# Kernel optimization log

Hardware: AMD Instinct MI355X
Metric: run time of the kernel (lower is better)

Reference implementation:

```python
import jax, jax.numpy as jnp
import numpy as np

M, N, P, D = 256, 512, 24, 8


def _se(X, Y):
    # base squared-exponential kernel between point sets: exp(-0.5*||x-y||^2)
    d2 = jnp.sum(X * X, -1)[:, None] + jnp.sum(Y * Y, -1)[None, :] - 2.0 * (X @ Y.T)
    return jnp.exp(-0.5 * jnp.maximum(d2, 0.0))


def _pairwise_dist(X1, A1, X2, A2):
    # vectorized version of the original double loop over metric(f1, f2)
    m, p, d = X1.shape
    n, q, _ = X2.shape
    # cross terms: C[i,j] = a_i @ K(x_i, x_j) @ a_j   (one big Gram, batched quadratic form)
    K12 = _se(X1.reshape(m * p, d), X2.reshape(n * q, d)).reshape(m, p, n, q)
    C = jnp.einsum('iu,iujv,jv->ij', A1, K12, A2)
    # self terms: s_i = a_i @ K(x_i, x_i) @ a_i (computed ONCE, not per inner iteration)
    s1 = jnp.einsum('iu,iuv,iv->i', A1, jax.vmap(_se)(X1, X1), A1)
    s2 = jnp.einsum('ju,juv,jv->j', A2, jax.vmap(_se)(X2, X2), A2)
    d2 = s1[:, None] + s2[None, :] - 2.0 * C
    # matches lax.cond(d2 <= 0, 0.0, sqrt(d2))
    return jnp.sqrt(jnp.maximum(d2, 0.0))


def _kernel(rho, X1, A1, X2, A2):
    # SquaredExponential profile applied to d / sqrt(rho)
    u = _pairwise_dist(X1, A1, X2, A2) / jnp.sqrt(rho)
    return jnp.exp(-0.5 * u * u)


def setup_inputs() -> dict:
    key = jax.random.key(0)
    k = jax.random.split(key, 5)
    return {
        'X_test': jax.random.normal(k[0], (M, P, D), jnp.float32),
        'A_test': 0.2 * jax.random.normal(k[1], (M, P), jnp.float32),
        'X_obs': jax.random.normal(k[2], (N, P, D), jnp.float32),
        'A_obs': 0.2 * jax.random.normal(k[3], (N, P), jnp.float32),
        'observed_ys': jax.random.normal(k[4], (N,), jnp.float32),
        'rho': jnp.asarray(4.0, jnp.float32),
        'g': jnp.asarray(1e-3, jnp.float32),
        'nu': jnp.asarray(1.0, jnp.float32),
        'b': jnp.asarray(0.0, jnp.float32),
    }


def reference(X_test, A_test, X_obs, A_obs, observed_ys, rho, g, nu, b):
    # predict(): Kxx, Kox, Koo then gp_posterior
    Kxx = nu * _kernel(rho, X_test, A_test, X_test, A_test)          # [M, M]
    Kox = nu * _kernel(rho, X_obs, A_obs, X_test, A_test)            # [N, M]
    Koo = nu * (_kernel(rho, X_obs, A_obs, X_obs, A_obs) + g * jnp.eye(N, dtype=X_obs.dtype))

    gain = jnp.linalg.solve(Koo, Kox).T                              # [M, N]
    mean = b + gain @ (observed_ys - b)                              # [M]
    cov = Kxx - gain @ Kox                                           # [M, M]
    Kbx = jnp.ones((1, N), Koo.dtype) @ gain.T                       # [1, M]
    # 1^T Koo^{-1} 1 == inv(Koo).sum(), computed via a solve
    Koo_inv_sum = jnp.linalg.solve(Koo, jnp.ones((N,), Koo.dtype)).sum()
    cov = cov + (1.0 - Kbx).T @ (1.0 - Kbx) / Koo_inv_sum
    # stack mean on top of cov -> [M+1, M]
    return jnp.concatenate([mean[None, :], cov], axis=0)
```

## Files before the change

kernel.cpp:

```cpp
#include <hip/hip_runtime.h>
#include <cmath>

#define M 256
#define N 512
#define P 24
#define D 8

__global__ __launch_bounds__(64) void self_kernel(const float* __restrict__ X_test,
                                                  const float* __restrict__ A_test,
                                                  const float* __restrict__ X_obs,
                                                  const float* __restrict__ A_obs,
                                                  float* __restrict__ s1,
                                                  float* __restrict__ s2,
                                                  float* __restrict__ atT,
                                                  float* __restrict__ atO,
                                                  double* __restrict__ Bc) {
    const int bid = blockIdx.x;
    const int lane = threadIdx.x;
    if (bid == M + N) {
#pragma unroll
        for (int t = 0; t < 8; ++t) Bc[(size_t)256 * 512 + 64 * t + lane] = 1.0;
        return;
    }
    const float* X; const float* A; float* s; float* at; int i;
    if (bid < M) { X = X_test; A = A_test; s = s1; at = atT; i = bid; }
    else         { X = X_obs;  A = A_obs;  s = s2; at = atO; i = bid - M; }
    const float* Xi = X + (size_t)i * P * D;
    const float* Ai = A + (size_t)i * P;
    float acc = 0.f;
#pragma unroll
    for (int t = 0; t < 9; ++t) {
        int idx = lane + 64 * t;
        int u = idx / 24;
        int v = idx - u * 24;
        const float* xu = Xi + u * D;
        const float* xv = Xi + v * D;
        float d2 = 0.f;
#pragma unroll
        for (int d = 0; d < D; ++d) { float df = xu[d] - xv[d]; d2 = fmaf(df, df, d2); }
        acc = fmaf(Ai[u] * Ai[v], __expf(-0.5f * d2), acc);
    }
#pragma unroll
    for (int off = 1; off < 64; off <<= 1) acc += __shfl_xor(acc, off, 64);
    if (lane == 0) s[i] = acc;
    if (lane < 24) {
        const float* xp = Xi + lane * D;
        float q = 0.f;
#pragma unroll
        for (int d = 0; d < D; ++d) q = fmaf(xp[d], xp[d], q);
        at[(size_t)i * P + lane] = Ai[lane] * __expf(-0.5f * q);
    }
}

__global__ __launch_bounds__(128) void gram_kernel(
    const float* __restrict__ Xt, const float* __restrict__ atT, const float* __restrict__ s1,
    const float* __restrict__ Xo, const float* __restrict__ atO, const float* __restrict__ s2,
    const float* __restrict__ rho_p, const float* __restrict__ nu_p, const float* __restrict__ g_p,
    float* __restrict__ Kox, float* __restrict__ Kxx, double* __restrict__ Koo,
    double* __restrict__ Bc) {
    const int mode = blockIdx.z;
    const int it = blockIdx.x, jt = blockIdx.y;
    const float *X1, *AT1, *S1, *X2, *AT2, *S2;
    if (mode == 0) {
        if (jt > 2 * it + 1) return;
        X1 = Xo; AT1 = atO; S1 = s2; X2 = Xo; AT2 = atO; S2 = s2;
    } else if (mode == 1) {
        if (jt >= 32) return;
        X1 = Xo; AT1 = atO; S1 = s2; X2 = Xt; AT2 = atT; S2 = s1;
    } else {
        if (it >= 16 || jt >= 32 || jt < 2 * it) return;
        X1 = Xt; AT1 = atT; S1 = s1; X2 = Xt; AT2 = atT; S2 = s1;
    }
    const int i0 = it * 16, j0 = jt * 8;
    const int tid = threadIdx.x;
    const int il = tid >> 3, uc = tid & 7;
    const int i = i0 + il;

    __shared__ __align__(16) float X2s[8 * 192];
    __shared__ float A2s[8 * 24];
    __shared__ float S2s[8];
    {
        const float4* gx = (const float4*)(X2 + (size_t)j0 * 192);
        float4* lx = (float4*)X2s;
        for (int idx = tid; idx < 8 * 48; idx += 128) lx[idx] = gx[idx];
        for (int idx = tid; idx < 8 * 24; idx += 128) A2s[idx] = AT2[(size_t)j0 * 24 + idx];
        if (tid < 8) S2s[tid] = S2[j0 + tid];
    }
    __syncthreads();

    float x1r[3][8], at1r[3];
#pragma unroll
    for (int ss = 0; ss < 3; ++ss) {
        const float* p = X1 + ((size_t)i * P + uc * 3 + ss) * D;
#pragma unroll
        for (int d = 0; d < D; ++d) x1r[ss][d] = p[d];
        at1r[ss] = AT1[(size_t)i * P + uc * 3 + ss];
    }
    const float s1i = S1[i];
    const float rho = rho_p[0], nu = nu_p[0], g = g_p[0];

    for (int jj = 0; jj < 8; ++jj) {
        const float* xb = X2s + jj * 192;
        float e0 = 0.f, e1 = 0.f, e2 = 0.f;
#pragma unroll 4
        for (int v = 0; v < 24; ++v) {
            const float4 q0 = ((const float4*)(xb + v * 8))[0];
            const float4 q1 = ((const float4*)(xb + v * 8))[1];
            float x2r[8];
            x2r[0] = q0.x; x2r[1] = q0.y; x2r[2] = q0.z; x2r[3] = q0.w;
            x2r[4] = q1.x; x2r[5] = q1.y; x2r[6] = q1.z; x2r[7] = q1.w;
            const float w2 = A2s[jj * 24 + v];
            float d0 = 0.f, d1 = 0.f, d2 = 0.f;
#pragma unroll
            for (int dd = 0; dd < 8; ++dd) {
                d0 = fmaf(x1r[0][dd], x2r[dd], d0);
                d1 = fmaf(x1r[1][dd], x2r[dd], d1);
                d2 = fmaf(x1r[2][dd], x2r[dd], d2);
            }
            e0 = fmaf(w2, __expf(d0), e0);
            e1 = fmaf(w2, __expf(d1), e1);
            e2 = fmaf(w2, __expf(d2), e2);
        }
        float acc = at1r[0] * e0;
        acc = fmaf(at1r[1], e1, acc);
        acc = fmaf(at1r[2], e2, acc);
        acc += __shfl_xor(acc, 1, 8);
        acc += __shfl_xor(acc, 2, 8);
        acc += __shfl_xor(acc, 4, 8);
        if (uc == 0) {
            const int j = j0 + jj;
            float d2p = fmaxf(s1i + S2s[jj] - 2.f * acc, 0.f);
            float kv = __expf(-0.5f * d2p / rho);
            if (mode == 0) {
                if (j <= i) Koo[(size_t)i * 512 + j] = (double)(nu * (kv + ((i == j) ? g : 0.f)));
            } else if (mode == 1) {
                float val = nu * kv;
                Kox[(size_t)i * 256 + j] = val;
                Bc[(size_t)j * 512 + i] = (double)val;
            } else {
                float val = nu * kv;
                if (j >= i) {
                    Kxx[(size_t)i * 256 + j] = val;
                    if (j > i) Kxx[(size_t)j * 256 + i] = val;
                }
            }
        }
    }
}

#define NT_(p) (7 - (p))
#define NS_(p) ((7 - (p)) * (8 - (p)) / 2)

__device__ __forceinline__ void spin_ge(int* f, int target) {
    if (threadIdx.x == 0) {
        while (__hip_atomic_load(f, __ATOMIC_ACQUIRE, __HIP_MEMORY_SCOPE_AGENT) < target)
            __builtin_amdgcn_s_sleep(2);
    }
    __syncthreads();
}

__global__ __launch_bounds__(256) void chol_kernel(double* __restrict__ A,
                                                   double* __restrict__ LT,
                                                   double* __restrict__ Dinv,
                                                   double* __restrict__ DinvT,
                                                   int* __restrict__ flags) {
    int* fdone = flags;
    int* tdone = flags + 8;
    int* s00   = flags + 16;
    int* scol0 = flags + 24;
    int* sall  = flags + 32;

    int bid = blockIdx.x, p = 0, rem = bid;
    for (;; ++p) {
        int tot = 1 + NT_(p) + NS_(p);
        if (rem < tot) break;
        rem -= tot;
    }
    const int k0 = p * 64;
    const int tid = threadIdx.x;

    __shared__ double smem[2 * 64 * 65 + 3 * 16 * 17];

    if (rem == 0) {
        double (*sA)[65] = (double(*)[65])smem;
        double (*sX)[65] = (double(*)[65])(smem + 64 * 65);
        double* sW = smem + 2 * 64 * 65;
        if (p > 0) spin_ge(&s00[p - 1], 1);
        for (int idx = tid; idx < 4096; idx += 256) {
            int r = idx >> 6, c = idx & 63;
            sA[r][c] = (c <= r) ? A[(size_t)(k0 + r) * 512 + k0 + c] : 0.0;
            sX[r][c] = 0.0;
        }
        __syncthreads();
        for (int q = 0; q < 4; ++q) {
            const int b0 = 16 * q;
            if (tid < 64) {
                for (int k = 0; k < 15; ++k) {
                    double inv = 1.0 / sA[b0 + k][b0 + k];
#pragma unroll
                    for (int t = 0; t < 4; ++t) {
                        int idx = tid + 64 * t, r = idx >> 4, c = idx & 15;
                        if (r > k && c > k && c <= r)
                            sA[b0 + r][b0 + c] -= sA[b0 + r][b0 + k] * sA[b0 + c][b0 + k] * inv;
                    }
                    asm volatile("" ::: "memory");
                }
                double dq = (tid < 16) ? sqrt(sA[b0 + tid][b0 + tid]) : 1.0;
                asm volatile("" ::: "memory");
#pragma unroll
                for (int t = 0; t < 4; ++t) {
                    int idx = tid + 64 * t, r = idx >> 4, c = idx & 15;
                    double dcol = __shfl(dq, c, 64);
                    if (c <= r) sA[b0 + r][b0 + c] = (r == c) ? dcol : sA[b0 + r][b0 + c] / dcol;
                }
                asm volatile("" ::: "memory");
                int c = tid >> 2, qd = tid & 3;
                if (qd == 0) sX[b0 + c][b0 + c] = 1.0 / sA[b0 + c][b0 + c];
                asm volatile("" ::: "memory");
                for (int r = 1; r < 16; ++r) {
                    double partial = 0.0;
                    for (int t = c + qd; t < r; t += 4)
                        partial = fma(sA[b0 + r][b0 + t], sX[b0 + t][b0 + c], partial);
                    partial += __shfl_xor(partial, 1, 4);
                    partial += __shfl_xor(partial, 2, 4);
                    if (qd == 0 && r > c)
                        sX[b0 + r][b0 + c] = -partial / sA[b0 + r][b0 + r];
                    asm volatile("" ::: "memory");
                }
            }
            __syncthreads();
            if (q < 3) {
                const int nrows = 48 - b0;
                const int cells = nrows * 16;
                double tv[3];
#pragma unroll
                for (int ii = 0; ii < 3; ++ii) {
                    int idx = tid + 256 * ii;
                    tv[ii] = 0.0;
                    if (idx < cells) {
                        int a = b0 + 16 + (idx >> 4), cc = idx & 15;
                        double acc = 0.0;
                        for (int t = 0; t <= cc; ++t)
                            acc = fma(sA[a][b0 + t], sX[b0 + cc][b0 + t], acc);
                        tv[ii] = acc;
                    }
                }
                __syncthreads();
#pragma unroll
                for (int ii = 0; ii < 3; ++ii) {
                    int idx = tid + 256 * ii;
                    if (idx < cells) {
                        int a = b0 + 16 + (idx >> 4), cc = idx & 15;
                        sA[a][b0 + cc] = tv[ii];
                    }
                }
                __syncthreads();
                for (int idx = tid; idx < nrows * nrows; idx += 256) {
                    int r = b0 + 16 + idx / nrows, cc = b0 + 16 + idx % nrows;
                    if (cc <= r) {
                        double acc = 0.0;
#pragma unroll
                        for (int t = 0; t < 16; ++t)
                            acc = fma(sA[r][b0 + t], sA[cc][b0 + t], acc);
                        sA[r][cc] -= acc;
                    }
                }
                __syncthreads();
            }
        }
        for (int d = 1; d <= 3; ++d) {
            __syncthreads();
            int npairs = 4 - d;
            for (int i2 = tid; i2 < npairs * 256; i2 += 256) {
                int pr = i2 >> 8, cell = i2 & 255, r = cell >> 4, c = cell & 15;
                int qc = pr, qr = pr + d;
                double w = 0.0;
                for (int t = 16 * qc; t < 16 * qr; ++t)
                    w = fma(sA[16 * qr + r][t], sX[t][16 * qc + c], w);
                sW[pr * 272 + r * 17 + c] = w;
            }
            __syncthreads();
            for (int i2 = tid; i2 < npairs * 256; i2 += 256) {
                int pr = i2 >> 8, cell = i2 & 255, r = cell >> 4, c = cell & 15;
                int qc = pr, qr = pr + d;
                double x = 0.0;
                for (int t = 0; t <= r; ++t)
                    x = fma(sX[16 * qr + r][16 * qr + t], sW[pr * 272 + t * 17 + c], x);
                sX[16 * qr + r][16 * qc + c] = -x;
            }
        }
        __syncthreads();
        for (int idx = tid; idx < 4096; idx += 256) {
            int r = idx >> 6, c = idx & 63;
            if (c <= r) {
                double lv = sA[r][c];
                A[(size_t)(k0 + r) * 512 + k0 + c] = lv;
                LT[(size_t)(k0 + c) * 512 + k0 + r] = lv;
            }
            double xv = sX[r][c];
            Dinv[(size_t)p * 4096 + idx] = xv;
            DinvT[(size_t)p * 4096 + (size_t)c * 64 + r] = xv;
        }
        __syncthreads();
        if (tid == 0) __hip_atomic_fetch_add(&fdone[p], 1, __ATOMIC_RELEASE, __HIP_MEMORY_SCOPE_AGENT);

    } else if (rem <= NT_(p)) {
        double (*sA)[65] = (double(*)[65])smem;
        double (*sB)[65] = (double(*)[65])(smem + 64 * 65);
        const int b = rem - 1;
        const int i0 = k0 + 64 + b * 64;
        if (p > 0) spin_ge(&scol0[p - 1], NT_(p - 1));
        spin_ge(&fdone[p], 1);
        for (int idx = tid; idx < 4096; idx += 256) {
            int r = idx >> 6, c = idx & 63;
            sA[r][c] = A[(size_t)(i0 + r) * 512 + k0 + c];
            sB[r][c] = DinvT[(size_t)p * 4096 + idx];
        }
        __syncthreads();
        const int tx = tid & 15, ty = tid >> 4;
        double acc[4][4] = {};
        for (int t = 0; t < 64; ++t) {
            double a0 = sA[4 * ty + 0][t], a1 = sA[4 * ty + 1][t];
            double a2 = sA[4 * ty + 2][t], a3 = sA[4 * ty + 3][t];
            double b0 = sB[t][4 * tx + 0], b1 = sB[t][4 * tx + 1];
            double b2 = sB[t][4 * tx + 2], b3 = sB[t][4 * tx + 3];
            acc[0][0] = fma(a0, b0, acc[0][0]); acc[0][1] = fma(a0, b1, acc[0][1]);
            acc[0][2] = fma(a0, b2, acc[0][2]); acc[0][3] = fma(a0, b3, acc[0][3]);
            acc[1][0] = fma(a1, b0, acc[1][0]); acc[1][1] = fma(a1, b1, acc[1][1]);
            acc[1][2] = fma(a1, b2, acc[1][2]); acc[1][3] = fma(a1, b3, acc[1][3]);
            acc[2][0] = fma(a2, b0, acc[2][0]); acc[2][1] = fma(a2, b1, acc[2][1]);
            acc[2][2] = fma(a2, b2, acc[2][2]); acc[2][3] = fma(a2, b3, acc[2][3]);
            acc[3][0] = fma(a3, b0, acc[3][0]); acc[3][1] = fma(a3, b1, acc[3][1]);
            acc[3][2] = fma(a3, b2, acc[3][2]); acc[3][3] = fma(a3, b3, acc[3][3]);
        }
#pragma unroll
        for (int r = 0; r < 4; ++r)
#pragma unroll
            for (int c = 0; c < 4; ++c) {
                A[(size_t)(i0 + 4 * ty + r) * 512 + k0 + 4 * tx + c] = acc[r][c];
                LT[(size_t)(k0 + 4 * tx + c) * 512 + i0 + 4 * ty + r] = acc[r][c];
            }
        __syncthreads();
        if (tid == 0) __hip_atomic_fetch_add(&tdone[p], 1, __ATOMIC_RELEASE, __HIP_MEMORY_SCOPE_AGENT);

    } else {
        double (*Li)[65] = (double(*)[65])smem;
        double (*Lj)[65] = (double(*)[65])(smem + 64 * 65);
        int s = rem - 1 - NT_(p);
        int bi = 0;
        while (s >= (bi + 1) * (bi + 2) / 2) ++bi;
        int bj = s - bi * (bi + 1) / 2;
        const int i0 = k0 + 64 + bi * 64, j0 = k0 + 64 + bj * 64;
        if (p > 0) spin_ge(&sall[p - 1], NS_(p - 1));
        spin_ge(&tdone[p], NT_(p));
        for (int idx = tid; idx < 4096; idx += 256) {
            int r = idx >> 6, c = idx & 63;
            Li[r][c] = A[(size_t)(i0 + r) * 512 + k0 + c];
            Lj[r][c] = A[(size_t)(j0 + r) * 512 + k0 + c];
        }
        __syncthreads();
        const int tx = tid & 15, ty = tid >> 4;
        double acc[4][4] = {};
        for (int t = 0; t < 64; ++t) {
            double a0 = Li[4 * ty + 0][t], a1 = Li[4 * ty + 1][t];
            double a2 = Li[4 * ty + 2][t], a3 = Li[4 * ty + 3][t];
            double b0 = Lj[4 * tx + 0][t], b1 = Lj[4 * tx + 1][t];
            double b2 = Lj[4 * tx + 2][t], b3 = Lj[4 * tx + 3][t];
            acc[0][0] = fma(a0, b0, acc[0][0]); acc[0][1] = fma(a0, b1, acc[0][1]);
            acc[0][2] = fma(a0, b2, acc[0][2]); acc[0][3] = fma(a0, b3, acc[0][3]);
            acc[1][0] = fma(a1, b0, acc[1][0]); acc[1][1] = fma(a1, b1, acc[1][1]);
            acc[1][2] = fma(a1, b2, acc[1][2]); acc[1][3] = fma(a1, b3, acc[1][3]);
            acc[2][0] = fma(a2, b0, acc[2][0]); acc[2][1] = fma(a2, b1, acc[2][1]);
            acc[2][2] = fma(a2, b2, acc[2][2]); acc[2][3] = fma(a2, b3, acc[2][3]);
            acc[3][0] = fma(a3, b0, acc[3][0]); acc[3][1] = fma(a3, b1, acc[3][1]);
            acc[3][2] = fma(a3, b2, acc[3][2]); acc[3][3] = fma(a3, b3, acc[3][3]);
        }
#pragma unroll
        for (int r = 0; r < 4; ++r)
#pragma unroll
            for (int c = 0; c < 4; ++c) {
                int gi = i0 + 4 * ty + r, gj = j0 + 4 * tx + c;
                if (bi != bj || gj <= gi) A[(size_t)gi * 512 + gj] -= acc[r][c];
            }
        __syncthreads();
        if (tid == 0) {
            __hip_atomic_fetch_add(&sall[p], 1, __ATOMIC_RELEASE, __HIP_MEMORY_SCOPE_AGENT);
            if (bj == 0) __hip_atomic_fetch_add(&scol0[p], 1, __ATOMIC_RELEASE, __HIP_MEMORY_SCOPE_AGENT);
            if (bi == 0 && bj == 0) __hip_atomic_fetch_add(&s00[p], 1, __ATOMIC_RELEASE, __HIP_MEMORY_SCOPE_AGENT);
        }
    }
}

__global__ __launch_bounds__(64) void solve_kernel(const double* __restrict__ L,
                                                   const double* __restrict__ U,
                                                   const double* __restrict__ Dinv,
                                                   const double* __restrict__ DinvT,
                                                   double* __restrict__ B,
                                                   const float* __restrict__ ys,
                                                   const float* __restrict__ b_p,
                                                   float* __restrict__ out,
                                                   double* __restrict__ kbx,
                                                   double* __restrict__ Sp) {
    const int c = blockIdx.x, lane = threadIdx.x;
    double* col = B + (size_t)c * 512;
    __shared__ double y[512];
    __shared__ double z[512];
    __shared__ double v[64];
    double breg[8];
#pragma unroll
    for (int k = 0; k < 8; ++k) breg[k] = col[64 * k + lane];
    for (int k = 0; k < 8; ++k) {
        const double* row = L + (size_t)(64 * k + lane) * 512;
        double acc = 0.0;
        for (int j = 0; j < 64 * k; j += 8) {
            double2 l0 = *(const double2*)(row + j + 0);
            double2 l1 = *(const double2*)(row + j + 2);
            double2 l2 = *(const double2*)(row + j + 4);
            double2 l3 = *(const double2*)(row + j + 6);
            acc = fma(l0.x, y[j + 0], acc); acc = fma(l0.y, y[j + 1], acc);
            acc = fma(l1.x, y[j + 2], acc); acc = fma(l1.y, y[j + 3], acc);
            acc = fma(l2.x, y[j + 4], acc); acc = fma(l2.y, y[j + 5], acc);
            acc = fma(l3.x, y[j + 6], acc); acc = fma(l3.y, y[j + 7], acc);
        }
        v[lane] = breg[k] - acc;
        __syncthreads();
        const double* Dk = DinvT + (size_t)k * 4096;
        double yr = 0.0;
#pragma unroll 8
        for (int t = 0; t < 64; ++t) yr = fma(Dk[t * 64 + lane], v[t], yr);
        y[64 * k + lane] = yr;
        __syncthreads();
    }
    for (int k = 7; k >= 0; --k) {
        const double* row = U + (size_t)(64 * k + lane) * 512;
        double acc = 0.0;
        for (int j = 64 * (k + 1); j < 512; j += 8) {
            double2 l0 = *(const double2*)(row + j + 0);
            double2 l1 = *(const double2*)(row + j + 2);
            double2 l2 = *(const double2*)(row + j + 4);
            double2 l3 = *(const double2*)(row + j + 6);
            acc = fma(l0.x, z[j + 0], acc); acc = fma(l0.y, z[j + 1], acc);
            acc = fma(l1.x, z[j + 2], acc); acc = fma(l1.y, z[j + 3], acc);
            acc = fma(l2.x, z[j + 4], acc); acc = fma(l2.y, z[j + 5], acc);
            acc = fma(l3.x, z[j + 6], acc); acc = fma(l3.y, z[j + 7], acc);
        }
        v[lane] = y[64 * k + lane] - acc;
        __syncthreads();
        const double* Dk = Dinv + (size_t)k * 4096;
        double zr = 0.0;
#pragma unroll 8
        for (int t = 0; t < 64; ++t) zr = fma(Dk[t * 64 + lane], v[t], zr);
        z[64 * k + lane] = zr;
        __syncthreads();
    }
    const double b = (double)b_p[0];
    double s0 = 0.0, s1 = 0.0;
#pragma unroll
    for (int k = 0; k < 8; ++k) {
        int n = 64 * k + lane;
        double zv = z[n];
        col[n] = zv;
        s0 += zv;
        s1 = fma(zv, (double)ys[n] - b, s1);
    }
#pragma unroll
    for (int off = 1; off < 64; off <<= 1) {
        s0 += __shfl_xor(s0, off, 64);
        s1 += __shfl_xor(s1, off, 64);
    }
    if (lane == 0) {
        if (c < 256) { out[c] = (float)(b + s1); kbx[c] = s0; }
        else Sp[0] = s0;
    }
}

__global__ __launch_bounds__(256) void cov_kernel(const double* __restrict__ Z,
                                                  const float* __restrict__ Kox,
                                                  const float* __restrict__ Kxx,
                                                  const double* __restrict__ kbx,
                                                  const double* __restrict__ Sp,
                                                  float* __restrict__ out) {
    const int bj = blockIdx.x, bi = blockIdx.y;
    const int tx = threadIdx.x & 15, ty = threadIdx.x >> 4;
    const int i = bi * 16 + ty, j = bj * 16 + tx;
    __shared__ double sZ[16][17];
    __shared__ float sK[16][17];
    double acc = 0.0;
    for (int kt = 0; kt < 32; ++kt) {
        sZ[ty][tx] = Z[(size_t)i * 512 + kt * 16 + tx];
        sK[ty][tx] = Kox[(size_t)(kt * 16 + ty) * 256 + j];
        __syncthreads();
#pragma unroll
        for (int t = 0; t < 16; ++t) acc = fma(sZ[ty][t], (double)sK[t][tx], acc);
        __syncthreads();
    }
    const double S = Sp[0];
    const double corr = (1.0 - kbx[i]) * (1.0 - kbx[j]) / S;
    out[(size_t)(1 + i) * 256 + j] = (float)((double)Kxx[(size_t)i * 256 + j] - acc + corr);
}

extern "C" void kernel_launch(void* const* d_in, const int* in_sizes, int n_in,
                              void* d_out, int out_size, void* d_ws, size_t ws_size,
                              hipStream_t stream) {
    const float* X_test = (const float*)d_in[0];
    const float* A_test = (const float*)d_in[1];
    const float* X_obs  = (const float*)d_in[2];
    const float* A_obs  = (const float*)d_in[3];
    const float* ys     = (const float*)d_in[4];
    const float* rho_p  = (const float*)d_in[5];
    const float* g_p    = (const float*)d_in[6];
    const float* nu_p   = (const float*)d_in[7];
    const float* b_p    = (const float*)d_in[8];
    float* out = (float*)d_out;
    char* ws = (char*)d_ws;

    double* Koo  = (double*)(ws + 0);
    double* LT   = (double*)(ws + 2097152);
    double* Bc   = (double*)(ws + 4194304);
    float*  Kox  = (float*) (ws + 5246976);
    float*  Kxx  = (float*) (ws + 5771264);
    float*  s1v  = (float*) (ws + 6033408);
    float*  s2v  = (float*) (ws + 6034432);
    double* kbx  = (double*)(ws + 6036480);
    double* Sp   = (double*)(ws + 6038528);
    int*    flags= (int*)   (ws + 6038784);
    double* Dinv = (double*)(ws + 6039552);
    double* DinvT= (double*)(ws + 6301696);
    float*  atT  = (float*)(ws + 2097152);
    float*  atO  = (float*)(ws + 2097152 + 24576);

    hipMemsetAsync(flags, 0, 192, stream);

    self_kernel<<<M + N + 1, 64, 0, stream>>>(X_test, A_test, X_obs, A_obs,
                                              s1v, s2v, atT, atO, Bc);

    gram_kernel<<<dim3(32, 64, 3), 128, 0, stream>>>(X_test, atT, s1v,
                                                     X_obs, atO, s2v,
                                                     rho_p, nu_p, g_p,
                                                     Kox, Kxx, Koo, Bc);

    chol_kernel<<<120, 256, 0, stream>>>(Koo, LT, Dinv, DinvT, flags);

    solve_kernel<<<257, 64, 0, stream>>>(Koo, LT, Dinv, DinvT, Bc, ys, b_p, out, kbx, Sp);

    cov_kernel<<<dim3(16, 16), 256, 0, stream>>>(Bc, Kox, Kxx, kbx, Sp, out);
}
```

Measured before the change: 1.012 ms.

## Replace spin-flag persistent Cholesky with per-panel kernel launches and fused updates

The single persistent Cholesky kernel, which coordinated stages through atomic spin-wait flags, is replaced by one diagonal-factor kernel followed by seven update launches. Each update launch recomputes the panel block (L times Dinv) inside every trailing block and fuses the next diagonal factorization into the (0,0) block. This removes spin-waiting, the flag memset and the separate triangular-solve tile stage. In exchange it adds launch overhead, duplicates the panel multiply across blocks, and leaves the next diagonal factorization running in a single serial block. The forward solve now reads the transposed factor with strided column loads instead of contiguous row vectors, which may coalesce worse.

```diff
diff --git a/kernel.cpp b/kernel.cpp
--- a/kernel.cpp
+++ b/kernel.cpp
@@ -148,251 +148,254 @@
     }
 }
 
-#define NT_(p) (7 - (p))
-#define NS_(p) ((7 - (p)) * (8 - (p)) / 2)
-
-__device__ __forceinline__ void spin_ge(int* f, int target) {
-    if (threadIdx.x == 0) {
-        while (__hip_atomic_load(f, __ATOMIC_ACQUIRE, __HIP_MEMORY_SCOPE_AGENT) < target)
-            __builtin_amdgcn_s_sleep(2);
+__device__ void factor64(double (*sA)[65], double (*sX)[65], double* sW,
+                         double* __restrict__ LT,
+                         double* __restrict__ Dinv,
+                         double* __restrict__ DinvT,
+                         int p) {
+    const int tid = threadIdx.x;
+    const int k0 = p * 64;
+    {
+        double* f = &sX[0][0];
+        for (int idx = tid; idx < 64 * 65; idx += 256) f[idx] = 0.0;
     }
     __syncthreads();
-}
-
-__global__ __launch_bounds__(256) void chol_kernel(double* __restrict__ A,
-                                                   double* __restrict__ LT,
-                                                   double* __restrict__ Dinv,
-                                                   double* __restrict__ DinvT,
-                                                   int* __restrict__ flags) {
-    int* fdone = flags;
-    int* tdone = flags + 8;
-    int* s00   = flags + 16;
-    int* scol0 = flags + 24;
-    int* sall  = flags + 32;
-
-    int bid = blockIdx.x, p = 0, rem = bid;
-    for (;; ++p) {
-        int tot = 1 + NT_(p) + NS_(p);
-        if (rem < tot) break;
-        rem -= tot;
-    }
-    const int k0 = p * 64;
-    const int tid = threadIdx.x;
-
-    __shared__ double smem[2 * 64 * 65 + 3 * 16 * 17];
-
-    if (rem == 0) {
-        double (*sA)[65] = (double(*)[65])smem;
-        double (*sX)[65] = (double(*)[65])(smem + 64 * 65);
-        double* sW = smem + 2 * 64 * 65;
-        if (p > 0) spin_ge(&s00[p - 1], 1);
-        for (int idx = tid; idx < 4096; idx += 256) {
-            int r = idx >> 6, c = idx & 63;
-            sA[r][c] = (c <= r) ? A[(size_t)(k0 + r) * 512 + k0 + c] : 0.0;
-            sX[r][c] = 0.0;
-        }
-        __syncthreads();
-        for (int q = 0; q < 4; ++q) {
-            const int b0 = 16 * q;
-            if (tid < 64) {
-                for (int k = 0; k < 15; ++k) {
-                    double inv = 1.0 / sA[b0 + k][b0 + k];
-#pragma unroll
-                    for (int t = 0; t < 4; ++t) {
-                        int idx = tid + 64 * t, r = idx >> 4, c = idx & 15;
-                        if (r > k && c > k && c <= r)
-                            sA[b0 + r][b0 + c] -= sA[b0 + r][b0 + k] * sA[b0 + c][b0 + k] * inv;
-                    }
-                    asm volatile("" ::: "memory");
-                }
-                double dq = (tid < 16) ? sqrt(sA[b0 + tid][b0 + tid]) : 1.0;
-                asm volatile("" ::: "memory");
+    for (int q = 0; q < 4; ++q) {
+        const int b0 = 16 * q;
+        if (tid < 64) {
+            for (int k = 0; k < 15; ++k) {
+                double inv = 1.0 / sA[b0 + k][b0 + k];
 #pragma unroll
                 for (int t = 0; t < 4; ++t) {
                     int idx = tid + 64 * t, r = idx >> 4, c = idx & 15;
-                    double dcol = __shfl(dq, c, 64);
-                    if (c <= r) sA[b0 + r][b0 + c] = (r == c) ? dcol : sA[b0 + r][b0 + c] / dcol;
+                    if (r > k && c > k && c <= r)
+                        sA[b0 + r][b0 + c] -= sA[b0 + r][b0 + k] * sA[b0 + c][b0 + k] * inv;
                 }
                 asm volatile("" ::: "memory");
-                int c = tid >> 2, qd = tid & 3;
-                if (qd == 0) sX[b0 + c][b0 + c] = 1.0 / sA[b0 + c][b0 + c];
+            }
+            double dq = (tid < 16) ? sqrt(sA[b0 + tid][b0 + tid]) : 1.0;
+            asm volatile("" ::: "memory");
+#pragma unroll
+            for (int t = 0; t < 4; ++t) {
+                int idx = tid + 64 * t, r = idx >> 4, c = idx & 15;
+                double dcol = __shfl(dq, c, 64);
+                if (c <= r) sA[b0 + r][b0 + c] = (r == c) ? dcol : sA[b0 + r][b0 + c] / dcol;
+            }
+            asm volatile("" ::: "memory");
+            int c = tid >> 2, qd = tid & 3;
+            if (qd == 0) sX[b0 + c][b0 + c] = 1.0 / sA[b0 + c][b0 + c];
+            asm volatile("" ::: "memory");
+            for (int r = 1; r < 16; ++r) {
+                double partial = 0.0;
+                for (int t = c + qd; t < r; t += 4)
+                    partial = fma(sA[b0 + r][b0 + t], sX[b0 + t][b0 + c], partial);
+                partial += __shfl_xor(partial, 1, 4);
+                partial += __shfl_xor(partial, 2, 4);
+                if (qd == 0 && r > c)
+                    sX[b0 + r][b0 + c] = -partial / sA[b0 + r][b0 + r];
                 asm volatile("" ::: "memory");
-                for (int r = 1; r < 16; ++r) {
-                    double partial = 0.0;
-                    for (int t = c + qd; t < r; t += 4)
-                        partial = fma(sA[b0 + r][b0 + t], sX[b0 + t][b0 + c], partial);
-                    partial += __shfl_xor(partial, 1, 4);
-                    partial += __shfl_xor(partial, 2, 4);
-                    if (qd == 0 && r > c)
-                        sX[b0 + r][b0 + c] = -partial / sA[b0 + r][b0 + r];
-                    asm volatile("" ::: "memory");
+            }
+        }
+        __syncthreads();
+        if (q < 3) {
+            const int nrows = 48 - b0;
+            const int cells = nrows * 16;
+            double tv[3];
+#pragma unroll
+            for (int ii = 0; ii < 3; ++ii) {
+                int idx = tid + 256 * ii;
+                tv[ii] = 0.0;
+                if (idx < cells) {
+                    int a = b0 + 16 + (idx >> 4), cc = idx & 15;
+                    double acc = 0.0;
+                    for (int t = 0; t <= cc; ++t)
+                        acc = fma(sA[a][b0 + t], sX[b0 + cc][b0 + t], acc);
+                    tv[ii] = acc;
                 }
             }
             __syncthreads();
-            if (q < 3) {
-                const int nrows = 48 - b0;
-                const int cells = nrows * 16;
-                double tv[3];
-#pragma unroll
-                for (int ii = 0; ii < 3; ++ii) {
-                    int idx = tid + 256 * ii;
-                    tv[ii] = 0.0;
-                    if (idx < cells) {
-                        int a = b0 + 16 + (idx >> 4), cc = idx & 15;
-                        double acc = 0.0;
-                        for (int t = 0; t <= cc; ++t)
-                            acc = fma(sA[a][b0 + t], sX[b0 + cc][b0 + t], acc);
-                        tv[ii] = acc;
-                    }
+#pragma unroll
+            for (int ii = 0; ii < 3; ++ii) {
+                int idx = tid + 256 * ii;
+                if (idx < cells) {
+                    int a = b0 + 16 + (idx >> 4), cc = idx & 15;
+                    sA[a][b0 + cc] = tv[ii];
                 }
-                __syncthreads();
-#pragma unroll
-                for (int ii = 0; ii < 3; ++ii) {
-                    int idx = tid + 256 * ii;
-                    if (idx < cells) {
-                        int a = b0 + 16 + (idx >> 4), cc = idx & 15;
-                        sA[a][b0 + cc] = tv[ii];
-                    }
+            }
+            __syncthreads();
+            for (int idx = tid; idx < nrows * nrows; idx += 256) {
+                int r = b0 + 16 + idx / nrows, cc = b0 + 16 + idx % nrows;
+                if (cc <= r) {
+                    double acc = 0.0;
+#pragma unroll
+                    for (int t = 0; t < 16; ++t)
+                        acc = fma(sA[r][b0 + t], sA[cc][b0 + t], acc);
+                    sA[r][cc] -= acc;
                 }
-                __syncthreads();
-                for (int idx = tid; idx < nrows * nrows; idx += 256) {
-                    int r = b0 + 16 + idx / nrows, cc = b0 + 16 + idx % nrows;
-                    if (cc <= r) {
-                        double acc = 0.0;
-#pragma unroll
-                        for (int t = 0; t < 16; ++t)
-                            acc = fma(sA[r][b0 + t], sA[cc][b0 + t], acc);
-                        sA[r][cc] -= acc;
-                    }
-                }
-                __syncthreads();
-            }
-        }
-        for (int d = 1; d <= 3; ++d) {
+            }
             __syncthreads();
-            int npairs = 4 - d;
-            for (int i2 = tid; i2 < npairs * 256; i2 += 256) {
-                int pr = i2 >> 8, cell = i2 & 255, r = cell >> 4, c = cell & 15;
-                int qc = pr, qr = pr + d;
-                double w = 0.0;
-                for (int t = 16 * qc; t < 16 * qr; ++t)
-                    w = fma(sA[16 * qr + r][t], sX[t][16 * qc + c], w);
-                sW[pr * 272 + r * 17 + c] = w;
-            }
-            __syncthreads();
-            for (int i2 = tid; i2 < npairs * 256; i2 += 256) {
-                int pr = i2 >> 8, cell = i2 & 255, r = cell >> 4, c = cell & 15;
-                int qc = pr, qr = pr + d;
-                double x = 0.0;
-                for (int t = 0; t <= r; ++t)
-                    x = fma(sX[16 * qr + r][16 * qr + t], sW[pr * 272 + t * 17 + c], x);
-                sX[16 * qr + r][16 * qc + c] = -x;
-            }
-        }
-        __syncthreads();
-        for (int idx = tid; idx < 4096; idx += 256) {
-            int r = idx >> 6, c = idx & 63;
-            if (c <= r) {
-                double lv = sA[r][c];
-                A[(size_t)(k0 + r) * 512 + k0 + c] = lv;
-                LT[(size_t)(k0 + c) * 512 + k0 + r] = lv;
-            }
-            double xv = sX[r][c];
-            Dinv[(size_t)p * 4096 + idx] = xv;
-            DinvT[(size_t)p * 4096 + (size_t)c * 64 + r] = xv;
-        }
-        __syncthreads();
-        if (tid == 0) __hip_atomic_fetch_add(&fdone[p], 1, __ATOMIC_RELEASE, __HIP_MEMORY_SCOPE_AGENT);
-
-    } else if (rem <= NT_(p)) {
-        double (*sA)[65] = (double(*)[65])smem;
-        double (*sB)[65] = (double(*)[65])(smem + 64 * 65);
-        const int b = rem - 1;
-        const int i0 = k0 + 64 + b * 64;
-        if (p > 0) spin_ge(&scol0[p - 1], NT_(p - 1));
-        spin_ge(&fdone[p], 1);
-        for (int idx = tid; idx < 4096; idx += 256) {
-            int r = idx >> 6, c = idx & 63;
-            sA[r][c] = A[(size_t)(i0 + r) * 512 + k0 + c];
-            sB[r][c] = DinvT[(size_t)p * 4096 + idx];
-        }
-        __syncthreads();
-        const int tx = tid & 15, ty = tid >> 4;
-        double acc[4][4] = {};
-        for (int t = 0; t < 64; ++t) {
-            double a0 = sA[4 * ty + 0][t], a1 = sA[4 * ty + 1][t];
-            double a2 = sA[4 * ty + 2][t], a3 = sA[4 * ty + 3][t];
-            double b0 = sB[t][4 * tx + 0], b1 = sB[t][4 * tx + 1];
-            double b2 = sB[t][4 * tx + 2], b3 = sB[t][4 * tx + 3];
-            acc[0][0] = fma(a0, b0, acc[0][0]); acc[0][1] = fma(a0, b1, acc[0][1]);
-            acc[0][2] = fma(a0, b2, acc[0][2]); acc[0][3] = fma(a0, b3, acc[0][3]);
-            acc[1][0] = fma(a1, b0, acc[1][0]); acc[1][1] = fma(a1, b1, acc[1][1]);
-            acc[1][2] = fma(a1, b2, acc[1][2]); acc[1][3] = fma(a1, b3, acc[1][3]);
-            acc[2][0] = fma(a2, b0, acc[2][0]); acc[2][1] = fma(a2, b1, acc[2][1]);
-            acc[2][2] = fma(a2, b2, acc[2][2]); acc[2][3] = fma(a2, b3, acc[2][3]);
-            acc[3][0] = fma(a3, b0, acc[3][0]); acc[3][1] = fma(a3, b1, acc[3][1]);
-            acc[3][2] = fma(a3, b2, acc[3][2]); acc[3][3] = fma(a3, b3, acc[3][3]);
-        }
+        }
+    }
+    for (int d = 1; d <= 3; ++d) {
+        __syncthreads();
+        int npairs = 4 - d;
+        for (int i2 = tid; i2 < npairs * 256; i2 += 256) {
+            int pr = i2 >> 8, cell = i2 & 255, r = cell >> 4, c = cell & 15;
+            int qc = pr, qr = pr + d;
+            double w = 0.0;
+            for (int t = 16 * qc; t < 16 * qr; ++t)
+                w = fma(sA[16 * qr + r][t], sX[t][16 * qc + c], w);
+            sW[pr * 272 + r * 17 + c] = w;
+        }
+        __syncthreads();
+        for (int i2 = tid; i2 < npairs * 256; i2 += 256) {
+            int pr = i2 >> 8, cell = i2 & 255, r = cell >> 4, c = cell & 15;
+            int qc = pr, qr = pr + d;
+            double x = 0.0;
+            for (int t = 0; t <= r; ++t)
+                x = fma(sX[16 * qr + r][16 * qr + t], sW[pr * 272 + t * 17 + c], x);
+            sX[16 * qr + r][16 * qc + c] = -x;
+        }
+    }
+    __syncthreads();
+    for (int idx = tid; idx < 4096; idx += 256) {
+        int r = idx >> 6, c = idx & 63;
+        if (c <= r) LT[(size_t)(k0 + c) * 512 + k0 + r] = sA[r][c];
+        double xv = sX[r][c];
+        Dinv[(size_t)p * 4096 + idx] = xv;
+        DinvT[(size_t)p * 4096 + (size_t)c * 64 + r] = xv;
+    }
+}
+
+__global__ __launch_bounds__(256) void factor0_kernel(const double* __restrict__ A,
+                                                      double* __restrict__ LT,
+                                                      double* __restrict__ Dinv,
+                                                      double* __restrict__ DinvT) {
+    __shared__ double smem[2 * 64 * 65 + 816];
+    double (*sA)[65] = (double(*)[65])smem;
+    double (*sX)[65] = (double(*)[65])(smem + 64 * 65);
+    double* sW = smem + 2 * 64 * 65;
+    const int tid = threadIdx.x;
+    for (int idx = tid; idx < 4096; idx += 256) {
+        int r = idx >> 6, c = idx & 63;
+        sA[r][c] = (c <= r) ? A[(size_t)r * 512 + c] : 0.0;
+    }
+    factor64(sA, sX, sW, LT, Dinv, DinvT, 0);
+}
+
+__global__ __launch_bounds__(256) void upd_kernel(double* __restrict__ A,
+                                                  double* __restrict__ LT,
+                                                  double* __restrict__ Dinv,
+                                                  double* __restrict__ DinvT,
+                                                  int p) {
+    __shared__ double smem[2 * 64 * 67 + 64 * 64];
+    double (*sLi)[67] = (double(*)[67])smem;
+    double (*sLj)[67] = (double(*)[67])(smem + 64 * 67);
+    double (*sD)[64]  = (double(*)[64])(smem + 2 * 64 * 67);
+
+    int s = blockIdx.x, bi = 0;
+    while (s >= bi + 1) { s -= bi + 1; ++bi; }
+    const int bj = s;
+    const int I = p + 1 + bi, J = p + 1 + bj;
+    const bool diag = (I == J);
+    const int tid = threadIdx.x;
+    const int tx = tid & 15, ty = tid >> 4;
+
+    const double* Ati = A + (size_t)I * 64 * 512 + (size_t)p * 64;
+    const double* Atj = A + (size_t)J * 64 * 512 + (size_t)p * 64;
+    for (int idx = tid; idx < 4096; idx += 256) {
+        int r = idx >> 6, c = idx & 63;
+        sLi[r][c] = Ati[(size_t)r * 512 + c];
+        if (!diag) sLj[r][c] = Atj[(size_t)r * 512 + c];
+        sD[r][c] = DinvT[(size_t)p * 4096 + idx];
+    }
+    __syncthreads();
+
+    double lip[4][4] = {}, ljp[4][4] = {};
+    for (int t = 0; t < 64; ++t) {
+        double b0 = sD[t][4 * tx + 0], b1 = sD[t][4 * tx + 1];
+        double b2 = sD[t][4 * tx + 2], b3 = sD[t][4 * tx + 3];
+#pragma unroll
+        for (int r = 0; r < 4; ++r) {
+            double a = sLi[4 * ty + r][t];
+            lip[r][0] = fma(a, b0, lip[r][0]);
+            lip[r][1] = fma(a, b1, lip[r][1]);
+            lip[r][2] = fma(a, b2, lip[r][2]);
+            lip[r][3] = fma(a, b3, lip[r][3]);
+        }
+        if (!diag) {
+#pragma unroll
+            for (int r = 0; r < 4; ++r) {
+                double a = sLj[4 * ty + r][t];
+                ljp[r][0] = fma(a, b0, ljp[r][0]);
+                ljp[r][1] = fma(a, b1, ljp[r][1]);
+                ljp[r][2] = fma(a, b2, ljp[r][2]);
+                ljp[r][3] = fma(a, b3, ljp[r][3]);
+            }
+        }
+    }
+    __syncthreads();
+#pragma unroll
+    for (int r = 0; r < 4; ++r)
+#pragma unroll
+        for (int c = 0; c < 4; ++c) {
+            sLi[4 * ty + r][4 * tx + c] = lip[r][c];
+            if (!diag) sLj[4 * ty + r][4 * tx + c] = ljp[r][c];
+        }
+    if (diag) {
 #pragma unroll
         for (int r = 0; r < 4; ++r)
 #pragma unroll
+            for (int c = 0; c < 4; ++c)
+                LT[(size_t)(p * 64 + 4 * tx + c) * 512 + (size_t)I * 64 + 4 * ty + r] = lip[r][c];
+    }
+    __syncthreads();
+
+    double (*Bp)[67] = diag ? sLi : sLj;
+    double acc[4][4] = {};
+    for (int t = 0; t < 64; ++t) {
+        double a0 = sLi[4 * ty + 0][t], a1 = sLi[4 * ty + 1][t];
+        double a2 = sLi[4 * ty + 2][t], a3 = sLi[4 * ty + 3][t];
+        double b0 = Bp[4 * tx + 0][t], b1 = Bp[4 * tx + 1][t];
+        double b2 = Bp[4 * tx + 2][t], b3 = Bp[4 * tx + 3][t];
+        acc[0][0] = fma(a0, b0, acc[0][0]); acc[0][1] = fma(a0, b1, acc[0][1]);
+        acc[0][2] = fma(a0, b2, acc[0][2]); acc[0][3] = fma(a0, b3, acc[0][3]);
+        acc[1][0] = fma(a1, b0, acc[1][0]); acc[1][1] = fma(a1, b1, acc[1][1]);
+        acc[1][2] = fma(a1, b2, acc[1][2]); acc[1][3] = fma(a1, b3, acc[1][3]);
+        acc[2][0] = fma(a2, b0, acc[2][0]); acc[2][1] = fma(a2, b1, acc[2][1]);
+        acc[2][2] = fma(a2, b2, acc[2][2]); acc[2][3] = fma(a2, b3, acc[2][3]);
+        acc[3][0] = fma(a3, b0, acc[3][0]); acc[3][1] = fma(a3, b1, acc[3][1]);
+        acc[3][2] = fma(a3, b2, acc[3][2]); acc[3][3] = fma(a3, b3, acc[3][3]);
+    }
+
+    double* Aij = A + (size_t)I * 64 * 512 + (size_t)J * 64;
+    if (bi == 0 && bj == 0) {
+        __syncthreads();
+        double (*fA)[65] = (double(*)[65])smem;
+        double (*fX)[65] = (double(*)[65])(smem + 64 * 65);
+        double* fW = smem + 2 * 64 * 65;
+#pragma unroll
+        for (int r = 0; r < 4; ++r)
+#pragma unroll
             for (int c = 0; c < 4; ++c) {
-                A[(size_t)(i0 + 4 * ty + r) * 512 + k0 + 4 * tx + c] = acc[r][c];
-                LT[(size_t)(k0 + 4 * tx + c) * 512 + i0 + 4 * ty + r] = acc[r][c];
-            }
-        __syncthreads();
-        if (tid == 0) __hip_atomic_fetch_add(&tdone[p], 1, __ATOMIC_RELEASE, __HIP_MEMORY_SCOPE_AGENT);
-
+                int rr = 4 * ty + r, cc = 4 * tx + c;
+                fA[rr][cc] = (cc <= rr) ? (Aij[(size_t)rr * 512 + cc] - acc[r][c]) : 0.0;
+            }
+        __syncthreads();
+        factor64(fA, fX, fW, LT, Dinv, DinvT, p + 1);
     } else {
-        double (*Li)[65] = (double(*)[65])smem;
-        double (*Lj)[65] = (double(*)[65])(smem + 64 * 65);
-        int s = rem - 1 - NT_(p);
-        int bi = 0;
-        while (s >= (bi + 1) * (bi + 2) / 2) ++bi;
-        int bj = s - bi * (bi + 1) / 2;
-        const int i0 = k0 + 64 + bi * 64, j0 = k0 + 64 + bj * 64;
-        if (p > 0) spin_ge(&sall[p - 1], NS_(p - 1));
-        spin_ge(&tdone[p], NT_(p));
-        for (int idx = tid; idx < 4096; idx += 256) {
-            int r = idx >> 6, c = idx & 63;
-            Li[r][c] = A[(size_t)(i0 + r) * 512 + k0 + c];
-            Lj[r][c] = A[(size_t)(j0 + r) * 512 + k0 + c];
-        }
-        __syncthreads();
-        const int tx = tid & 15, ty = tid >> 4;
-        double acc[4][4] = {};
-        for (int t = 0; t < 64; ++t) {
-            double a0 = Li[4 * ty + 0][t], a1 = Li[4 * ty + 1][t];
-            double a2 = Li[4 * ty + 2][t], a3 = Li[4 * ty + 3][t];
-            double b0 = Lj[4 * tx + 0][t], b1 = Lj[4 * tx + 1][t];
-            double b2 = Lj[4 * tx + 2][t], b3 = Lj[4 * tx + 3][t];
-            acc[0][0] = fma(a0, b0, acc[0][0]); acc[0][1] = fma(a0, b1, acc[0][1]);
-            acc[0][2] = fma(a0, b2, acc[0][2]); acc[0][3] = fma(a0, b3, acc[0][3]);
-            acc[1][0] = fma(a1, b0, acc[1][0]); acc[1][1] = fma(a1, b1, acc[1][1]);
-            acc[1][2] = fma(a1, b2, acc[1][2]); acc[1][3] = fma(a1, b3, acc[1][3]);
-            acc[2][0] = fma(a2, b0, acc[2][0]); acc[2][1] = fma(a2, b1, acc[2][1]);
-            acc[2][2] = fma(a2, b2, acc[2][2]); acc[2][3] = fma(a2, b3, acc[2][3]);
-            acc[3][0] = fma(a3, b0, acc[3][0]); acc[3][1] = fma(a3, b1, acc[3][1]);
-            acc[3][2] = fma(a3, b2, acc[3][2]); acc[3][3] = fma(a3, b3, acc[3][3]);
-        }
 #pragma unroll
         for (int r = 0; r < 4; ++r)
 #pragma unroll
             for (int c = 0; c < 4; ++c) {
-                int gi = i0 + 4 * ty + r, gj = j0 + 4 * tx + c;
-                if (bi != bj || gj <= gi) A[(size_t)gi * 512 + gj] -= acc[r][c];
-            }
-        __syncthreads();
-        if (tid == 0) {
-            __hip_atomic_fetch_add(&sall[p], 1, __ATOMIC_RELEASE, __HIP_MEMORY_SCOPE_AGENT);
-            if (bj == 0) __hip_atomic_fetch_add(&scol0[p], 1, __ATOMIC_RELEASE, __HIP_MEMORY_SCOPE_AGENT);
-            if (bi == 0 && bj == 0) __hip_atomic_fetch_add(&s00[p], 1, __ATOMIC_RELEASE, __HIP_MEMORY_SCOPE_AGENT);
-        }
-    }
-}
-
-__global__ __launch_bounds__(64) void solve_kernel(const double* __restrict__ L,
-                                                   const double* __restrict__ U,
+                int rr = 4 * ty + r, cc = 4 * tx + c;
+                if (!diag || cc <= rr)
+                    Aij[(size_t)rr * 512 + cc] -= acc[r][c];
+            }
+    }
+}
+
+__global__ __launch_bounds__(64) void solve_kernel(const double* __restrict__ U,
                                                    const double* __restrict__ Dinv,
                                                    const double* __restrict__ DinvT,
                                                    double* __restrict__ B,
@@ -410,17 +413,13 @@
 #pragma unroll
     for (int k = 0; k < 8; ++k) breg[k] = col[64 * k + lane];
     for (int k = 0; k < 8; ++k) {
-        const double* row = L + (size_t)(64 * k + lane) * 512;
         double acc = 0.0;
-        for (int j = 0; j < 64 * k; j += 8) {
-            double2 l0 = *(const double2*)(row + j + 0);
-            double2 l1 = *(const double2*)(row + j + 2);
-            double2 l2 = *(const double2*)(row + j + 4);
-            double2 l3 = *(const double2*)(row + j + 6);
-            acc = fma(l0.x, y[j + 0], acc); acc = fma(l0.y, y[j + 1], acc);
-            acc = fma(l1.x, y[j + 2], acc); acc = fma(l1.y, y[j + 3], acc);
-            acc = fma(l2.x, y[j + 4], acc); acc = fma(l2.y, y[j + 5], acc);
-            acc = fma(l3.x, y[j + 6], acc); acc = fma(l3.y, y[j + 7], acc);
+        const int base = 64 * k + lane;
+        const int jmax = 64 * k;
+        for (int j = 0; j < jmax; j += 8) {
+#pragma unroll
+            for (int u = 0; u < 8; ++u)
+                acc = fma(U[(size_t)(j + u) * 512 + base], y[j + u], acc);
         }
         v[lane] = breg[k] - acc;
         __syncthreads();
@@ -523,14 +522,11 @@
     float*  s2v  = (float*) (ws + 6034432);
     double* kbx  = (double*)(ws + 6036480);
     double* Sp   = (double*)(ws + 6038528);
-    int*    flags= (int*)   (ws + 6038784);
     double* Dinv = (double*)(ws + 6039552);
     double* DinvT= (double*)(ws + 6301696);
     float*  atT  = (float*)(ws + 2097152);
     float*  atO  = (float*)(ws + 2097152 + 24576);
 
-    hipMemsetAsync(flags, 0, 192, stream);
-
     self_kernel<<<M + N + 1, 64, 0, stream>>>(X_test, A_test, X_obs, A_obs,
                                               s1v, s2v, atT, atO, Bc);
 
@@ -539,9 +535,13 @@
                                                      rho_p, nu_p, g_p,
                                                      Kox, Kxx, Koo, Bc);
 
-    chol_kernel<<<120, 256, 0, stream>>>(Koo, LT, Dinv, DinvT, flags);
-
-    solve_kernel<<<257, 64, 0, stream>>>(Koo, LT, Dinv, DinvT, Bc, ys, b_p, out, kbx, Sp);
+    factor0_kernel<<<1, 256, 0, stream>>>(Koo, LT, Dinv, DinvT);
+    for (int p = 0; p < 7; ++p) {
+        int nb = (7 - p) * (8 - p) / 2;
+        upd_kernel<<<nb, 256, 0, stream>>>(Koo, LT, Dinv, DinvT, p);
+    }
+
+    solve_kernel<<<257, 64, 0, stream>>>(LT, Dinv, DinvT, Bc, ys, b_p, out, kbx, Sp);
 
     cov_kernel<<<dim3(16, 16), 256, 0, stream>>>(Bc, Kox, Kxx, kbx, Sp, out);
 }
```

New measurement: 1.061 ms. 4.8% more time.
